# Kernel optimization log

Hardware: AMD Instinct MI355X
Metric: run time of the kernel (lower is better)

## Reference

```python
import jax, jax.numpy as jnp
import numpy as np

DELTA_V = 0.5
DELTA_D = 3.0
NUM_LANES = 4  # instance labels are 0 (background) .. NUM_LANES


def setup_inputs() -> dict:
    key = jax.random.key(0)
    k1, k2, k3 = jax.random.split(key, 3)
    B, E, H, W = 16, 4, 512, 1024
    pred = jax.random.normal(k1, (B, E, H, W), dtype=jnp.float32)
    binary_label = jax.random.randint(k2, (B, H, W), 0, 2).astype(jnp.float32)
    instance_label = jax.random.randint(k3, (B, H, W), 0, NUM_LANES + 1).astype(jnp.int32)
    return {"pred": pred, "binary_label": binary_label, "instance_label": instance_label}


def _forward(pred, binary_label, instance_label):
    B, E, H, W = pred.shape
    N = H * W
    C = NUM_LANES
    # masked embedding: zero out background per the binary mask
    pr = (binary_label[:, None, :, :] * pred).reshape(B, E, N)  # [B,E,N]
    pr = jnp.swapaxes(pr, 1, 2).reshape(B * N, E)               # [B*N,E]
    seg = (jnp.arange(B, dtype=jnp.int32)[:, None] * (C + 1)
           + instance_label.reshape(B, N)).reshape(-1)          # [B*N]
    nseg = B * (C + 1)
    sums = jax.ops.segment_sum(pr, seg, num_segments=nseg).reshape(B, C + 1, E)[:, 1:]      # [B,C,E]
    sumsq = jax.ops.segment_sum(pr * pr, seg, num_segments=nseg).reshape(B, C + 1, E)[:, 1:]
    counts = jax.ops.segment_sum(jnp.ones((B * N,), pred.dtype), seg,
                                 num_segments=nseg).reshape(B, C + 1)[:, 1:]                # [B,C]
    mu = sums / counts[..., None]                                # [B,C,E] cluster means
    # ||xi - mu||_F^2 over all masked pixels and channels of cluster c
    ssd = jnp.maximum((sumsq - counts[..., None] * mu * mu).sum(-1), 0.0)  # [B,C]
    nrm = jnp.sqrt(ssd)
    var = jnp.where(nrm > DELTA_V, (nrm - DELTA_V) ** 2, 0.0)
    L_var = var.mean()  # mean over all B*C cluster terms (matches sum/len)
    # pairwise center repulsion, ordered pairs i != j (double-counted as in original)
    diff = mu[:, :, None, :] - mu[:, None, :, :]                 # [B,C,C,E]
    d2 = (diff * diff).sum(-1)                                   # [B,C,C]
    eye = jnp.eye(C, dtype=bool)
    dist = jnp.sqrt(jnp.where(eye, 1.0, d2))
    dloss = jnp.where(eye, 0.0, jax.nn.relu(DELTA_D - dist) ** 2).sum((-1, -2))  # [B]
    L_dist = dloss.mean()
    return L_var + L_dist


def reference(pred, binary_label, instance_label):
    return _forward(pred, binary_label, instance_label)
```

## Files before the change

kernel.cpp:

```cpp
#include <hip/hip_runtime.h>

#define NB 16
#define NE 4
#define NC 4
#define NH 512
#define NW 1024
#define NPIX (NH * NW)

constexpr int THREADS = 256;
constexpr int BLOCKS_PER_BATCH = 128;
constexpr int UNITS_PER_BATCH = NPIX / 4;
constexpr int ITERS = UNITS_PER_BATCH / (BLOCKS_PER_BATCH * THREADS);

#define WS_STRIDE 36

__global__ __launch_bounds__(THREADS) void accum_kernel(
    const float* __restrict__ pred,
    const float* __restrict__ mask,
    const int*   __restrict__ inst,
    float* __restrict__ ws)
{
    const int b   = blockIdx.y;
    const int bx  = blockIdx.x;
    const int tid = threadIdx.x;

    float s[NC][NE] = {};
    float q[NC][NE] = {};
    float n[NC]     = {};

    const float4* pm = reinterpret_cast<const float4*>(mask + (size_t)b * NPIX);
    const int4*   pi = reinterpret_cast<const int4*>(inst + (size_t)b * NPIX);
    const float4* pp0 = reinterpret_cast<const float4*>(pred + ((size_t)b * NE + 0) * NPIX);
    const float4* pp1 = reinterpret_cast<const float4*>(pred + ((size_t)b * NE + 1) * NPIX);
    const float4* pp2 = reinterpret_cast<const float4*>(pred + ((size_t)b * NE + 2) * NPIX);
    const float4* pp3 = reinterpret_cast<const float4*>(pred + ((size_t)b * NE + 3) * NPIX);

    #pragma unroll
    for (int k = 0; k < ITERS; ++k) {
        const int u = bx * (THREADS * ITERS) + k * THREADS + tid;
        const float4 m4 = pm[u];
        const int4   i4 = pi[u];
        float4 p4[NE];
        p4[0] = pp0[u]; p4[1] = pp1[u]; p4[2] = pp2[u]; p4[3] = pp3[u];

        #pragma unroll
        for (int j = 0; j < 4; ++j) {
            const float mm  = (&m4.x)[j];
            const int   lab = (&i4.x)[j];
            float v[NE], sq[NE];
            #pragma unroll
            for (int e = 0; e < NE; ++e) {
                const float x = mm * (&p4[e].x)[j];
                v[e]  = x;
                sq[e] = x * x;
            }
            #pragma unroll
            for (int c = 0; c < NC; ++c) {
                const float ind = (lab == c + 1) ? 1.0f : 0.0f;
                n[c] += ind;
                #pragma unroll
                for (int e = 0; e < NE; ++e) {
                    s[c][e] = fmaf(ind, v[e],  s[c][e]);
                    q[c][e] = fmaf(ind, sq[e], q[c][e]);
                }
            }
        }
    }

    #pragma unroll
    for (int c = 0; c < NC; ++c) {
        #pragma unroll
        for (int e = 0; e < NE; ++e) {
            #pragma unroll
            for (int off = 32; off; off >>= 1) {
                s[c][e] += __shfl_xor(s[c][e], off);
                q[c][e] += __shfl_xor(q[c][e], off);
            }
        }
        #pragma unroll
        for (int off = 32; off; off >>= 1) n[c] += __shfl_xor(n[c], off);
    }

    __shared__ float red[THREADS / 64][WS_STRIDE];
    const int wave = tid >> 6;
    const int lane = tid & 63;
    if (lane == 0) {
        float* dst = red[wave];
        #pragma unroll
        for (int c = 0; c < NC; ++c)
            #pragma unroll
            for (int e = 0; e < NE; ++e) {
                dst[c * 4 + e]      = s[c][e];
                dst[16 + c * 4 + e] = q[c][e];
            }
        #pragma unroll
        for (int c = 0; c < NC; ++c) dst[32 + c] = n[c];
    }
    __syncthreads();
    if (tid < WS_STRIDE) {
        float tot = red[0][tid] + red[1][tid] + red[2][tid] + red[3][tid];
        atomicAdd(&ws[b * WS_STRIDE + tid], tot);
    }
}

__global__ __launch_bounds__(64) void finalize_kernel(
    const float* __restrict__ ws, float* __restrict__ out)
{
    const int lane = threadIdx.x;
    const int b = lane >> 2;
    const int c = lane & 3;
    const float* wb = ws + b * WS_STRIDE;

    const float cnt = wb[32 + c];
    float mu[NE];
    float ssd = 0.0f;
    #pragma unroll
    for (int e = 0; e < NE; ++e) {
        const float sm = wb[c * 4 + e];
        const float qq = wb[16 + c * 4 + e];
        const float m  = sm / cnt;
        mu[e] = m;
        ssd += qq - cnt * m * m;
    }
    ssd = fmaxf(ssd, 0.0f);
    const float nrm = sqrtf(ssd);
    const float dv  = nrm - 0.5f;
    float var = (nrm > 0.5f) ? dv * dv : 0.0f;

    float dsum = 0.0f;
    const int base = lane & ~3;
    #pragma unroll
    for (int j = 0; j < NC; ++j) {
        float d2 = 0.0f;
        #pragma unroll
        for (int e = 0; e < NE; ++e) {
            const float mj = __shfl(mu[e], base + j);
            const float df = mu[e] - mj;
            d2 = fmaf(df, df, d2);
        }
        if (j != c) {
            const float dist = sqrtf(d2);
            const float r = fmaxf(3.0f - dist, 0.0f);
            dsum += r * r;
        }
    }

    #pragma unroll
    for (int off = 32; off; off >>= 1) {
        var  += __shfl_xor(var,  off);
        dsum += __shfl_xor(dsum, off);
    }
    if (lane == 0)
        out[0] = var / (float)(NB * NC) + dsum / (float)NB;
}

extern "C" void kernel_launch(void* const* d_in, const int* in_sizes, int n_in,
                              void* d_out, int out_size, void* d_ws, size_t ws_size,
                              hipStream_t stream) {
    const float* pred = (const float*)d_in[0];
    const float* mask = (const float*)d_in[1];
    const int*   inst = (const int*)d_in[2];
    float* out = (float*)d_out;
    float* ws  = (float*)d_ws;

    hipMemsetAsync(d_ws, 0, NB * WS_STRIDE * sizeof(float), stream);

    dim3 grid(BLOCKS_PER_BATCH, NB);
    accum_kernel<<<grid, THREADS, 0, stream>>>(pred, mask, inst, ws);
    finalize_kernel<<<1, 64, 0, stream>>>(ws, out);
}
```

Before: 244.3 us.

## Double-buffer loads, halve grid, drop atomics and memset for two-stage reduction

The accumulation kernel now prefetches the next iteration's mask, label and prediction vectors into a second register buffer, and the grid is halved so each thread handles twice as many units. The cross-lane reduction is cut to two shuffle steps, after which 64 partials per block are summed in shared memory. Per-block results go to distinct workspace slots instead of atomics, which removes the memset. A wider finalize kernel sums those slots. The extra double-buffer registers may lower occupancy on a purely memory-bound stream.

```diff
diff --git a/kernel.cpp b/kernel.cpp
--- a/kernel.cpp
+++ b/kernel.cpp
@@ -3,15 +3,12 @@
 #define NB 16
 #define NE 4
 #define NC 4
-#define NH 512
-#define NW 1024
-#define NPIX (NH * NW)
+#define NPIX (512 * 1024)
 
 constexpr int THREADS = 256;
-constexpr int BLOCKS_PER_BATCH = 128;
-constexpr int UNITS_PER_BATCH = NPIX / 4;
-constexpr int ITERS = UNITS_PER_BATCH / (BLOCKS_PER_BATCH * THREADS);
-
+constexpr int BPB     = 64;
+constexpr int UNITS   = NPIX / 4;
+constexpr int ITERS   = UNITS / (BPB * THREADS);
 #define WS_STRIDE 36
 
 __global__ __launch_bounds__(THREADS) void accum_kernel(
@@ -28,29 +25,38 @@
     float q[NC][NE] = {};
     float n[NC]     = {};
 
-    const float4* pm = reinterpret_cast<const float4*>(mask + (size_t)b * NPIX);
-    const int4*   pi = reinterpret_cast<const int4*>(inst + (size_t)b * NPIX);
+    const float4* pm  = reinterpret_cast<const float4*>(mask + (size_t)b * NPIX);
+    const int4*   pi  = reinterpret_cast<const int4*>(inst + (size_t)b * NPIX);
     const float4* pp0 = reinterpret_cast<const float4*>(pred + ((size_t)b * NE + 0) * NPIX);
     const float4* pp1 = reinterpret_cast<const float4*>(pred + ((size_t)b * NE + 1) * NPIX);
     const float4* pp2 = reinterpret_cast<const float4*>(pred + ((size_t)b * NE + 2) * NPIX);
     const float4* pp3 = reinterpret_cast<const float4*>(pred + ((size_t)b * NE + 3) * NPIX);
 
+    const int base = bx * (THREADS * ITERS) + tid;
+
+    float4 m4[2]; int4 i4[2]; float4 p[2][NE];
+    {
+        const int u = base;
+        m4[0] = pm[u]; i4[0] = pi[u];
+        p[0][0] = pp0[u]; p[0][1] = pp1[u]; p[0][2] = pp2[u]; p[0][3] = pp3[u];
+    }
+
     #pragma unroll
     for (int k = 0; k < ITERS; ++k) {
-        const int u = bx * (THREADS * ITERS) + k * THREADS + tid;
-        const float4 m4 = pm[u];
-        const int4   i4 = pi[u];
-        float4 p4[NE];
-        p4[0] = pp0[u]; p4[1] = pp1[u]; p4[2] = pp2[u]; p4[3] = pp3[u];
-
+        const int cur = k & 1, nxt = cur ^ 1;
+        if (k + 1 < ITERS) {
+            const int u = base + (k + 1) * THREADS;
+            m4[nxt] = pm[u]; i4[nxt] = pi[u];
+            p[nxt][0] = pp0[u]; p[nxt][1] = pp1[u]; p[nxt][2] = pp2[u]; p[nxt][3] = pp3[u];
+        }
         #pragma unroll
         for (int j = 0; j < 4; ++j) {
-            const float mm  = (&m4.x)[j];
-            const int   lab = (&i4.x)[j];
+            const float mm  = (&m4[cur].x)[j];
+            const int   lab = (&i4[cur].x)[j];
             float v[NE], sq[NE];
             #pragma unroll
             for (int e = 0; e < NE; ++e) {
-                const float x = mm * (&p4[e].x)[j];
+                const float x = mm * (&p[cur][e].x)[j];
                 v[e]  = x;
                 sq[e] = x * x;
             }
@@ -71,87 +77,100 @@
     for (int c = 0; c < NC; ++c) {
         #pragma unroll
         for (int e = 0; e < NE; ++e) {
-            #pragma unroll
-            for (int off = 32; off; off >>= 1) {
-                s[c][e] += __shfl_xor(s[c][e], off);
-                q[c][e] += __shfl_xor(q[c][e], off);
-            }
+            s[c][e] += __shfl_xor(s[c][e], 1); s[c][e] += __shfl_xor(s[c][e], 2);
+            q[c][e] += __shfl_xor(q[c][e], 1); q[c][e] += __shfl_xor(q[c][e], 2);
         }
-        #pragma unroll
-        for (int off = 32; off; off >>= 1) n[c] += __shfl_xor(n[c], off);
+        n[c] += __shfl_xor(n[c], 1); n[c] += __shfl_xor(n[c], 2);
     }
 
-    __shared__ float red[THREADS / 64][WS_STRIDE];
-    const int wave = tid >> 6;
-    const int lane = tid & 63;
-    if (lane == 0) {
-        float* dst = red[wave];
+    __shared__ float red[64][WS_STRIDE];
+    const int lane = tid & 63, wave = tid >> 6;
+    if ((lane & 3) == 0) {
+        float* dst = red[wave * 16 + (lane >> 2)];
         #pragma unroll
-        for (int c = 0; c < NC; ++c)
+        for (int c = 0; c < NC; ++c) {
             #pragma unroll
             for (int e = 0; e < NE; ++e) {
                 dst[c * 4 + e]      = s[c][e];
                 dst[16 + c * 4 + e] = q[c][e];
             }
-        #pragma unroll
-        for (int c = 0; c < NC; ++c) dst[32 + c] = n[c];
+            dst[32 + c] = n[c];
+        }
     }
     __syncthreads();
+
     if (tid < WS_STRIDE) {
-        float tot = red[0][tid] + red[1][tid] + red[2][tid] + red[3][tid];
-        atomicAdd(&ws[b * WS_STRIDE + tid], tot);
+        float tot = 0.0f;
+        #pragma unroll
+        for (int p2 = 0; p2 < 64; ++p2) tot += red[p2][tid];
+        ws[((size_t)(b * BPB + bx)) * WS_STRIDE + tid] = tot;
     }
 }
 
-__global__ __launch_bounds__(64) void finalize_kernel(
+constexpr int FT = 640;
+__global__ __launch_bounds__(FT) void finalize_kernel(
     const float* __restrict__ ws, float* __restrict__ out)
 {
-    const int lane = threadIdx.x;
-    const int b = lane >> 2;
-    const int c = lane & 3;
-    const float* wb = ws + b * WS_STRIDE;
+    __shared__ float fin[NB * WS_STRIDE];
+    const int t = threadIdx.x;
+    if (t < NB * WS_STRIDE) {
+        const int b = t / WS_STRIDE, v = t % WS_STRIDE;
+        float tot = 0.0f;
+        #pragma unroll 8
+        for (int blk = 0; blk < BPB; ++blk)
+            tot += ws[((size_t)(b * BPB + blk)) * WS_STRIDE + v];
+        fin[t] = tot;
+    }
+    __syncthreads();
 
-    const float cnt = wb[32 + c];
-    float mu[NE];
-    float ssd = 0.0f;
-    #pragma unroll
-    for (int e = 0; e < NE; ++e) {
-        const float sm = wb[c * 4 + e];
-        const float qq = wb[16 + c * 4 + e];
-        const float m  = sm / cnt;
-        mu[e] = m;
-        ssd += qq - cnt * m * m;
-    }
-    ssd = fmaxf(ssd, 0.0f);
-    const float nrm = sqrtf(ssd);
-    const float dv  = nrm - 0.5f;
-    float var = (nrm > 0.5f) ? dv * dv : 0.0f;
+    if (t < 64) {
+        const int lane = t;
+        const int b = lane >> 2;
+        const int c = lane & 3;
+        const float* wb = fin + b * WS_STRIDE;
 
-    float dsum = 0.0f;
-    const int base = lane & ~3;
-    #pragma unroll
-    for (int j = 0; j < NC; ++j) {
-        float d2 = 0.0f;
+        const float cnt = wb[32 + c];
+        float mu[NE];
+        float ssd = 0.0f;
         #pragma unroll
         for (int e = 0; e < NE; ++e) {
-            const float mj = __shfl(mu[e], base + j);
-            const float df = mu[e] - mj;
-            d2 = fmaf(df, df, d2);
+            const float sm = wb[c * 4 + e];
+            const float qq = wb[16 + c * 4 + e];
+            const float m  = sm / cnt;
+            mu[e] = m;
+            ssd += qq - cnt * m * m;
         }
-        if (j != c) {
-            const float dist = sqrtf(d2);
-            const float r = fmaxf(3.0f - dist, 0.0f);
-            dsum += r * r;
+        ssd = fmaxf(ssd, 0.0f);
+        const float nrm = sqrtf(ssd);
+        const float dv  = nrm - 0.5f;
+        float var = (nrm > 0.5f) ? dv * dv : 0.0f;
+
+        float dsum = 0.0f;
+        const int qbase = lane & ~3;
+        #pragma unroll
+        for (int j = 0; j < NC; ++j) {
+            float d2 = 0.0f;
+            #pragma unroll
+            for (int e = 0; e < NE; ++e) {
+                const float mj = __shfl(mu[e], qbase + j);
+                const float df = mu[e] - mj;
+                d2 = fmaf(df, df, d2);
+            }
+            if (j != c) {
+                const float dist = sqrtf(d2);
+                const float r = fmaxf(3.0f - dist, 0.0f);
+                dsum += r * r;
+            }
         }
+
+        #pragma unroll
+        for (int off = 32; off; off >>= 1) {
+            var  += __shfl_xor(var,  off);
+            dsum += __shfl_xor(dsum, off);
+        }
+        if (lane == 0)
+            out[0] = var / (float)(NB * NC) + dsum / (float)NB;
     }
-
-    #pragma unroll
-    for (int off = 32; off; off >>= 1) {
-        var  += __shfl_xor(var,  off);
-        dsum += __shfl_xor(dsum, off);
-    }
-    if (lane == 0)
-        out[0] = var / (float)(NB * NC) + dsum / (float)NB;
 }
 
 extern "C" void kernel_launch(void* const* d_in, const int* in_sizes, int n_in,
@@ -163,9 +182,7 @@
     float* out = (float*)d_out;
     float* ws  = (float*)d_ws;
 
-    hipMemsetAsync(d_ws, 0, NB * WS_STRIDE * sizeof(float), stream);
-
-    dim3 grid(BLOCKS_PER_BATCH, NB);
+    dim3 grid(BPB, NB);
     accum_kernel<<<grid, THREADS, 0, stream>>>(pred, mask, inst, ws);
-    finalize_kernel<<<1, 64, 0, stream>>>(ws, out);
+    finalize_kernel<<<1, FT, 0, stream>>>(ws, out);
 }
```

New measurement: 241.1 us. About the same (-1.3%).
